# Kernel tuning notes

Measured on AMD Instinct MI355X. Metric: run time of the kernel, lower is better.

Reference implementation:

```python
import jax, jax.numpy as jnp
import numpy as np

C_IN = 256
C_INTER = C_IN // 2  # max(1, C//2)
B, D, H, W = 2, 16, 64, 64


def setup_inputs() -> dict:
    key = jax.random.key(0)
    ks = jax.random.split(key, 9)
    s = 1.0 / np.sqrt(C_IN)
    si = 1.0 / np.sqrt(C_INTER)
    return {
        "x": jax.random.normal(ks[0], (B, C_IN, D, H, W), dtype=jnp.float32),
        # 1x1x1 conv weights reduce to [out, in] matrices
        "g_w": jax.random.normal(ks[1], (C_INTER, C_IN), dtype=jnp.float32) * s,
        "g_b": jax.random.normal(ks[2], (C_INTER,), dtype=jnp.float32) * s,
        "theta_w": jax.random.normal(ks[3], (C_INTER, C_IN), dtype=jnp.float32) * s,
        "theta_b": jax.random.normal(ks[4], (C_INTER,), dtype=jnp.float32) * s,
        "phi_w": jax.random.normal(ks[5], (C_INTER, C_IN), dtype=jnp.float32) * s,
        "phi_b": jax.random.normal(ks[6], (C_INTER,), dtype=jnp.float32) * s,
        # note: torch code inits W to zero; random here so gradients/outputs are non-trivial
        "W_w": jax.random.normal(ks[7], (C_IN, C_INTER), dtype=jnp.float32) * si,
        "W_b": jax.random.normal(ks[8], (C_IN,), dtype=jnp.float32) * si,
    }


def reference(x, g_w, g_b, theta_w, theta_b, phi_w, phi_b, W_w, W_b):
    b, c, d, h, w = x.shape
    n = d * h * w
    xf = x.reshape(b, c, n)  # [B, C, N]
    # 1x1x1 convs == per-position linear projections
    g = jnp.einsum('oc,bcn->bon', g_w, xf) + g_b[None, :, None]        # [B, Ci, N]
    th = jnp.einsum('oc,bcn->bon', theta_w, xf) + theta_b[None, :, None]
    ph = jnp.einsum('oc,bcn->bon', phi_w, xf) + phi_b[None, :, None]
    # f = theta^T @ phi (N x N), y = (f / N) @ g^T. Since the normalizer is a
    # constant, reassociate: kv = phi @ g^T is [Ci, Ci], avoiding the NxN matrix.
    kv = jnp.einsum('bin,bjn->bij', ph, g)                              # [B, Ci, Ci]
    y = jnp.einsum('bin,bij->bjn', th, kv) / n                          # [B, Ci, N]
    y = jnp.einsum('oc,bcn->bon', W_w, y) + W_b[None, :, None]          # [B, C, N]
    return x + y.reshape(b, c, d, h, w)
```

## Files before the change

kernel.cpp:

```cpp
#include <hip/hip_runtime.h>

#define NB 2
#define CC 256
#define CI 128
#define NN 65536
#define KSPLIT 64
#define KCHUNK 1024
#define STAGE 64
#define LDA 72
#define LDX 264

typedef __bf16 bf16x8 __attribute__((ext_vector_type(8)));
typedef float f32x4 __attribute__((ext_vector_type(4)));

__device__ __forceinline__ unsigned short f2bf(float f) {
  unsigned u = __float_as_uint(f);
  u += 0x7fffu + ((u >> 16) & 1u);
  return (unsigned short)(u >> 16);
}

__global__ __launch_bounds__(256) void nl3d_syrk(const float* __restrict__ x,
                                                 float* __restrict__ S,
                                                 float* __restrict__ svec) {
  __shared__ unsigned short ldsA[128 * LDA];
  __shared__ unsigned short ldsB[128 * LDA];
  const int tid = threadIdx.x;
  const int lane = tid & 63;
  const int wv = tid >> 6;
  const int wm = wv >> 1, wn = wv & 1;
  const int b = blockIdx.z;
  const int pair = blockIdx.y;
  const int I = (pair == 2) ? 1 : 0;
  const int J = (pair == 0) ? 0 : 1;
  const bool diag = (I == J);
  const int kc0 = blockIdx.x * KCHUNK;

  const float* xb = x + (size_t)b * CC * NN;
  f32x4 acc[4][4];
  const f32x4 zero4 = {0.f, 0.f, 0.f, 0.f};
#pragma unroll
  for (int i = 0; i < 4; ++i)
#pragma unroll
    for (int j = 0; j < 4; ++j) acc[i][j] = zero4;

  float rsum[8];
#pragma unroll
  for (int i = 0; i < 8; ++i) rsum[i] = 0.f;

  const int rA = tid >> 4;
  const int c4 = tid & 15;
  unsigned short* ldsBp = diag ? ldsA : ldsB;

  for (int s = 0; s < KCHUNK / STAGE; ++s) {
    const int kc = kc0 + s * STAGE;
    float4 fa[8], fb[8];
#pragma unroll
    for (int i = 0; i < 8; ++i) {
      int row = i * 16 + rA;
      fa[i] = *(const float4*)(xb + (size_t)(I * 128 + row) * NN + kc + c4 * 4);
    }
    if (!diag) {
#pragma unroll
      for (int i = 0; i < 8; ++i) {
        int row = i * 16 + rA;
        fb[i] = *(const float4*)(xb + (size_t)(J * 128 + row) * NN + kc + c4 * 4);
      }
    }
    __syncthreads();
#pragma unroll
    for (int i = 0; i < 8; ++i) {
      int row = i * 16 + rA;
      ushort4 h;
      h.x = f2bf(fa[i].x); h.y = f2bf(fa[i].y); h.z = f2bf(fa[i].z); h.w = f2bf(fa[i].w);
      *(ushort4*)&ldsA[row * LDA + c4 * 4] = h;
      if (diag) rsum[i] += fa[i].x + fa[i].y + fa[i].z + fa[i].w;
    }
    if (!diag) {
#pragma unroll
      for (int i = 0; i < 8; ++i) {
        int row = i * 16 + rA;
        ushort4 h;
        h.x = f2bf(fb[i].x); h.y = f2bf(fb[i].y); h.z = f2bf(fb[i].z); h.w = f2bf(fb[i].w);
        *(ushort4*)&ldsB[row * LDA + c4 * 4] = h;
      }
    }
    __syncthreads();

    const int m = lane & 15;
    const int kg = (lane >> 4) * 8;
#pragma unroll
    for (int kk = 0; kk < 2; ++kk) {
      bf16x8 afr[4], bfr[4];
#pragma unroll
      for (int mt = 0; mt < 4; ++mt)
        afr[mt] = *(const bf16x8*)&ldsA[(wm * 64 + mt * 16 + m) * LDA + kk * 32 + kg];
#pragma unroll
      for (int nt = 0; nt < 4; ++nt)
        bfr[nt] = *(const bf16x8*)&ldsBp[(wn * 64 + nt * 16 + m) * LDA + kk * 32 + kg];
#pragma unroll
      for (int mt = 0; mt < 4; ++mt)
#pragma unroll
        for (int nt = 0; nt < 4; ++nt)
          acc[mt][nt] = __builtin_amdgcn_mfma_f32_16x16x32_bf16(afr[mt], bfr[nt], acc[mt][nt], 0, 0, 0);
    }
  }

  {
    float* Sb = S + (size_t)b * CC * CC;
    const int col = lane & 15;
    const int rquad = (lane >> 4) * 4;
#pragma unroll
    for (int mt = 0; mt < 4; ++mt)
#pragma unroll
      for (int nt = 0; nt < 4; ++nt)
#pragma unroll
        for (int r = 0; r < 4; ++r) {
          int gi = I * 128 + wm * 64 + mt * 16 + rquad + r;
          int gj = J * 128 + wn * 64 + nt * 16 + col;
          float v = acc[mt][nt][r];
          atomicAdd(&Sb[gi * CC + gj], v);
          if (!diag) atomicAdd(&Sb[gj * CC + gi], v);
        }
  }

  if (diag) {
    __syncthreads();
    float* ldsRS = (float*)ldsA;
    if (tid < 128) ldsRS[tid] = 0.f;
    __syncthreads();
#pragma unroll
    for (int i = 0; i < 8; ++i) atomicAdd(&ldsRS[i * 16 + rA], rsum[i]);
    __syncthreads();
    if (tid < 128) atomicAdd(&svec[b * CC + I * 128 + tid], ldsRS[tid]);
  }
}

__global__ void nl3d_b0(const float* __restrict__ g_w, float* __restrict__ gwT) {
  int t = blockIdx.x * 256 + threadIdx.x;
  int j = t >> 8, d = t & 255;
  gwT[d * CI + j] = g_w[t];
}

__global__ void nl3d_b1(const float* __restrict__ phi_w, const float* __restrict__ S,
                        float* __restrict__ P) {
  int b = blockIdx.x >> 7, i = blockIdx.x & 127, d = threadIdx.x;
  const float* Sb = S + (size_t)b * CC * CC;
  float acc = 0.f;
  for (int c = 0; c < CC; ++c) acc += phi_w[i * CC + c] * Sb[c * CC + d];
  P[((size_t)b * CI + i) * CC + d] = acc;
}

__global__ void nl3d_b2(const float* __restrict__ P, const float* __restrict__ gwT,
                        const float* __restrict__ svec, const float* __restrict__ phi_w,
                        const float* __restrict__ phi_b, const float* __restrict__ g_b,
                        float* __restrict__ kv) {
  int b = blockIdx.x >> 7, i = blockIdx.x & 127, j = threadIdx.x;
  const float* Pr = P + ((size_t)b * CI + i) * CC;
  const float* sv = svec + b * CC;
  float u = 0.f;
  for (int c = 0; c < CC; ++c) u += phi_w[i * CC + c] * sv[c];
  float acc = 0.f, v = 0.f;
  for (int d = 0; d < CC; ++d) {
    float gT = gwT[d * CI + j];
    acc += Pr[d] * gT;
    v += sv[d] * gT;
  }
  kv[((size_t)b * CI + i) * CI + j] = acc + u * g_b[j] + phi_b[i] * (v + (float)NN * g_b[j]);
}

__global__ void nl3d_b3(const float* __restrict__ kv, const float* __restrict__ theta_w,
                        const float* __restrict__ theta_b, float* __restrict__ T2,
                        float* __restrict__ tb2) {
  int b = blockIdx.x >> 7, j = blockIdx.x & 127, c = threadIdx.x;
  const float* kvb = kv + (size_t)b * CI * CI;
  float acc = 0.f;
  for (int i = 0; i < CI; ++i) acc += kvb[i * CI + j] * theta_w[i * CC + c];
  T2[((size_t)b * CI + j) * CC + c] = acc;
  if (c == 0) {
    float t = 0.f;
    for (int i = 0; i < CI; ++i) t += kvb[i * CI + j] * theta_b[i];
    tb2[b * CI + j] = t;
  }
}

__global__ void nl3d_b4(const float* __restrict__ T2, const float* __restrict__ tb2,
                        const float* __restrict__ W_w, const float* __restrict__ W_b,
                        unsigned short* __restrict__ Mbf, float* __restrict__ cvec) {
  int b = blockIdx.x >> 8, o = blockIdx.x & 255, c = threadIdx.x;
  const float inv = 1.0f / (float)NN;
  float acc = 0.f;
  for (int j = 0; j < CI; ++j) acc += W_w[o * CI + j] * T2[((size_t)b * CI + j) * CC + c];
  Mbf[((size_t)b * CC + o) * CC + c] = f2bf(acc * inv);
  if (c == 0) {
    float t = 0.f;
    for (int j = 0; j < CI; ++j) t += W_w[o * CI + j] * tb2[b * CI + j];
    cvec[b * CC + o] = t * inv + W_b[o];
  }
}

__global__ __launch_bounds__(256) void nl3d_out(const float* __restrict__ x,
                                                const unsigned short* __restrict__ Mbf,
                                                const float* __restrict__ cvec,
                                                float* __restrict__ out) {
  __shared__ unsigned short xT[64 * LDX];
  const int tid = threadIdx.x;
  const int lane = tid & 63;
  const int wv = tid >> 6;
  const int b = blockIdx.y;
  const int n0 = blockIdx.x * 64;

  const float* xb = x + (size_t)b * CC * NN;
  float* ob = out + (size_t)b * CC * NN;

  {
    const int c4 = tid & 15;
#pragma unroll
    for (int i = 0; i < 8; ++i) {
      int p = i * 16 + (tid >> 4);
      float4 f0 = *(const float4*)(xb + (size_t)(2 * p) * NN + n0 + c4 * 4);
      float4 f1 = *(const float4*)(xb + (size_t)(2 * p + 1) * NN + n0 + c4 * 4);
      float a0[4] = {f0.x, f0.y, f0.z, f0.w};
      float a1[4] = {f1.x, f1.y, f1.z, f1.w};
#pragma unroll
      for (int j = 0; j < 4; ++j) {
        unsigned pack = (unsigned)f2bf(a0[j]) | ((unsigned)f2bf(a1[j]) << 16);
        *(unsigned*)&xT[(c4 * 4 + j) * LDX + 2 * p] = pack;
      }
    }
  }
  __syncthreads();

  f32x4 acc[4][4];
  const f32x4 zero4 = {0.f, 0.f, 0.f, 0.f};
#pragma unroll
  for (int i = 0; i < 4; ++i)
#pragma unroll
    for (int j = 0; j < 4; ++j) acc[i][j] = zero4;

  const int m = lane & 15;
  const int kg = (lane >> 4) * 8;
  const unsigned short* Mb = Mbf + (size_t)b * CC * CC;
#pragma unroll
  for (int kc = 0; kc < 8; ++kc) {
    bf16x8 afr[4], bfr[4];
#pragma unroll
    for (int mt = 0; mt < 4; ++mt)
      afr[mt] = *(const bf16x8*)(Mb + (size_t)(wv * 64 + mt * 16 + m) * CC + kc * 32 + kg);
#pragma unroll
    for (int nt = 0; nt < 4; ++nt)
      bfr[nt] = *(const bf16x8*)&xT[(nt * 16 + m) * LDX + kc * 32 + kg];
#pragma unroll
    for (int mt = 0; mt < 4; ++mt)
#pragma unroll
      for (int nt = 0; nt < 4; ++nt)
        acc[mt][nt] = __builtin_amdgcn_mfma_f32_16x16x32_bf16(afr[mt], bfr[nt], acc[mt][nt], 0, 0, 0);
  }

  const int col = lane & 15;
  const int rquad = (lane >> 4) * 4;
#pragma unroll
  for (int mt = 0; mt < 4; ++mt)
#pragma unroll
    for (int r = 0; r < 4; ++r) {
      int o = wv * 64 + mt * 16 + rquad + r;
      float cv = cvec[b * CC + o];
      const float* xrow = xb + (size_t)o * NN + n0;
      float* orow = ob + (size_t)o * NN + n0;
#pragma unroll
      for (int nt = 0; nt < 4; ++nt) {
        int n = nt * 16 + col;
        orow[n] = xrow[n] + acc[mt][nt][r] + cv;
      }
    }
}

extern "C" void kernel_launch(void* const* d_in, const int* in_sizes, int n_in,
                              void* d_out, int out_size, void* d_ws, size_t ws_size,
                              hipStream_t stream) {
  const float* x       = (const float*)d_in[0];
  const float* g_w     = (const float*)d_in[1];
  const float* g_b     = (const float*)d_in[2];
  const float* theta_w = (const float*)d_in[3];
  const float* theta_b = (const float*)d_in[4];
  const float* phi_w   = (const float*)d_in[5];
  const float* phi_b   = (const float*)d_in[6];
  const float* W_w     = (const float*)d_in[7];
  const float* W_b     = (const float*)d_in[8];
  float* out = (float*)d_out;

  char* ws = (char*)d_ws;
  float* S    = (float*)(ws);
  float* svec = (float*)(ws + 524288);
  float* P    = (float*)(ws + 526336);
  float* gwT  = (float*)(ws + 788480);
  float* kv   = (float*)(ws + 919552);
  float* T2   = (float*)(ws + 1050624);
  float* tb2  = (float*)(ws + 1312768);
  unsigned short* Mbf = (unsigned short*)(ws + 1313792);
  float* cvec = (float*)(ws + 1575936);

  hipMemsetAsync(ws, 0, 526336, stream);
  nl3d_syrk<<<dim3(KSPLIT, 3, NB), 256, 0, stream>>>(x, S, svec);
  nl3d_b0<<<128, 256, 0, stream>>>(g_w, gwT);
  nl3d_b1<<<NB * CI, 256, 0, stream>>>(phi_w, S, P);
  nl3d_b2<<<NB * CI, 128, 0, stream>>>(P, gwT, svec, phi_w, phi_b, g_b, kv);
  nl3d_b3<<<NB * CI, 256, 0, stream>>>(kv, theta_w, theta_b, T2, tb2);
  nl3d_b4<<<NB * CC, 256, 0, stream>>>(T2, tb2, W_w, W_b, Mbf, cvec);
  nl3d_out<<<dim3(NN / 64, NB), 256, 0, stream>>>(x, Mbf, cvec, out);
}
```

Baseline: 431.5 us.

## Compute full Gram matrix per block with partial-sum reduction and swizzled LDS

The Gram kernel now computes the full 256x256 product per block with 512 threads, instead of three 128x128 pair blocks, so each x tile is read once per block. When workspace allows, each split writes its partial sum to workspace and a separate kernel reduces them, replacing global atomics. The small matrix kernels use multiple accumulators to break dependency chains, and the output kernel XOR-swizzles its transposed LDS tile to cut bank conflicts. The full-matrix tile computes the symmetric half redundantly, uses more accumulator registers, and adds a partials write/read.

```diff
diff --git a/kernel.cpp b/kernel.cpp
--- a/kernel.cpp
+++ b/kernel.cpp
@@ -4,9 +4,6 @@
 #define CC 256
 #define CI 128
 #define NN 65536
-#define KSPLIT 64
-#define KCHUNK 1024
-#define STAGE 64
 #define LDA 72
 #define LDX 264
 
@@ -19,70 +16,51 @@
   return (unsigned short)(u >> 16);
 }
 
-__global__ __launch_bounds__(256) void nl3d_syrk(const float* __restrict__ x,
-                                                 float* __restrict__ S,
-                                                 float* __restrict__ svec) {
-  __shared__ unsigned short ldsA[128 * LDA];
-  __shared__ unsigned short ldsB[128 * LDA];
+__global__ __launch_bounds__(512) void nl3d_syrk2(const float* __restrict__ x,
+                                                  float* __restrict__ S,
+                                                  float* __restrict__ partials,
+                                                  float* __restrict__ svec,
+                                                  int kchunk, int use_partial) {
+  __shared__ unsigned short lds[256 * LDA];
   const int tid = threadIdx.x;
   const int lane = tid & 63;
   const int wv = tid >> 6;
-  const int wm = wv >> 1, wn = wv & 1;
-  const int b = blockIdx.z;
-  const int pair = blockIdx.y;
-  const int I = (pair == 2) ? 1 : 0;
-  const int J = (pair == 0) ? 0 : 1;
-  const bool diag = (I == J);
-  const int kc0 = blockIdx.x * KCHUNK;
+  const int wm = wv & 3, wn = wv >> 2;
+  const int b = blockIdx.y;
+  const int kc0 = blockIdx.x * kchunk;
 
   const float* xb = x + (size_t)b * CC * NN;
-  f32x4 acc[4][4];
+  f32x4 acc[4][8];
   const f32x4 zero4 = {0.f, 0.f, 0.f, 0.f};
 #pragma unroll
   for (int i = 0; i < 4; ++i)
 #pragma unroll
-    for (int j = 0; j < 4; ++j) acc[i][j] = zero4;
+    for (int j = 0; j < 8; ++j) acc[i][j] = zero4;
 
   float rsum[8];
 #pragma unroll
   for (int i = 0; i < 8; ++i) rsum[i] = 0.f;
 
-  const int rA = tid >> 4;
+  const int r0 = tid >> 4;
   const int c4 = tid & 15;
-  unsigned short* ldsBp = diag ? ldsA : ldsB;
-
-  for (int s = 0; s < KCHUNK / STAGE; ++s) {
-    const int kc = kc0 + s * STAGE;
-    float4 fa[8], fb[8];
+
+  const int stages = kchunk >> 6;
+  for (int s = 0; s < stages; ++s) {
+    const int kc = kc0 + s * 64;
+    float4 f[8];
 #pragma unroll
     for (int i = 0; i < 8; ++i) {
-      int row = i * 16 + rA;
-      fa[i] = *(const float4*)(xb + (size_t)(I * 128 + row) * NN + kc + c4 * 4);
-    }
-    if (!diag) {
-#pragma unroll
-      for (int i = 0; i < 8; ++i) {
-        int row = i * 16 + rA;
-        fb[i] = *(const float4*)(xb + (size_t)(J * 128 + row) * NN + kc + c4 * 4);
-      }
+      int row = r0 + 32 * i;
+      f[i] = *(const float4*)(xb + (size_t)row * NN + kc + c4 * 4);
     }
     __syncthreads();
 #pragma unroll
     for (int i = 0; i < 8; ++i) {
-      int row = i * 16 + rA;
+      int row = r0 + 32 * i;
       ushort4 h;
-      h.x = f2bf(fa[i].x); h.y = f2bf(fa[i].y); h.z = f2bf(fa[i].z); h.w = f2bf(fa[i].w);
-      *(ushort4*)&ldsA[row * LDA + c4 * 4] = h;
-      if (diag) rsum[i] += fa[i].x + fa[i].y + fa[i].z + fa[i].w;
-    }
-    if (!diag) {
-#pragma unroll
-      for (int i = 0; i < 8; ++i) {
-        int row = i * 16 + rA;
-        ushort4 h;
-        h.x = f2bf(fb[i].x); h.y = f2bf(fb[i].y); h.z = f2bf(fb[i].z); h.w = f2bf(fb[i].w);
-        *(ushort4*)&ldsB[row * LDA + c4 * 4] = h;
-      }
+      h.x = f2bf(f[i].x); h.y = f2bf(f[i].y); h.z = f2bf(f[i].z); h.w = f2bf(f[i].w);
+      *(ushort4*)&lds[row * LDA + c4 * 4] = h;
+      rsum[i] += f[i].x + f[i].y + f[i].z + f[i].w;
     }
     __syncthreads();
 
@@ -90,49 +68,76 @@
     const int kg = (lane >> 4) * 8;
 #pragma unroll
     for (int kk = 0; kk < 2; ++kk) {
-      bf16x8 afr[4], bfr[4];
+      bf16x8 afr[4], bfr[8];
 #pragma unroll
       for (int mt = 0; mt < 4; ++mt)
-        afr[mt] = *(const bf16x8*)&ldsA[(wm * 64 + mt * 16 + m) * LDA + kk * 32 + kg];
-#pragma unroll
-      for (int nt = 0; nt < 4; ++nt)
-        bfr[nt] = *(const bf16x8*)&ldsBp[(wn * 64 + nt * 16 + m) * LDA + kk * 32 + kg];
+        afr[mt] = *(const bf16x8*)&lds[(wm * 64 + mt * 16 + m) * LDA + kk * 32 + kg];
+#pragma unroll
+      for (int nt = 0; nt < 8; ++nt)
+        bfr[nt] = *(const bf16x8*)&lds[(wn * 128 + nt * 16 + m) * LDA + kk * 32 + kg];
 #pragma unroll
       for (int mt = 0; mt < 4; ++mt)
 #pragma unroll
-        for (int nt = 0; nt < 4; ++nt)
+        for (int nt = 0; nt < 8; ++nt)
           acc[mt][nt] = __builtin_amdgcn_mfma_f32_16x16x32_bf16(afr[mt], bfr[nt], acc[mt][nt], 0, 0, 0);
     }
   }
 
-  {
+  const int col = lane & 15;
+  const int rq = (lane >> 4) * 4;
+  if (use_partial) {
+    float* dst = partials + ((size_t)(b * gridDim.x + blockIdx.x)) * (CC * CC);
+#pragma unroll
+    for (int mt = 0; mt < 4; ++mt)
+#pragma unroll
+      for (int nt = 0; nt < 8; ++nt)
+#pragma unroll
+        for (int r = 0; r < 4; ++r) {
+          int gi = wm * 64 + mt * 16 + rq + r;
+          int gj = wn * 128 + nt * 16 + col;
+          dst[gi * CC + gj] = acc[mt][nt][r];
+        }
+  } else {
     float* Sb = S + (size_t)b * CC * CC;
-    const int col = lane & 15;
-    const int rquad = (lane >> 4) * 4;
 #pragma unroll
     for (int mt = 0; mt < 4; ++mt)
 #pragma unroll
-      for (int nt = 0; nt < 4; ++nt)
+      for (int nt = 0; nt < 8; ++nt)
 #pragma unroll
         for (int r = 0; r < 4; ++r) {
-          int gi = I * 128 + wm * 64 + mt * 16 + rquad + r;
-          int gj = J * 128 + wn * 64 + nt * 16 + col;
-          float v = acc[mt][nt][r];
-          atomicAdd(&Sb[gi * CC + gj], v);
-          if (!diag) atomicAdd(&Sb[gj * CC + gi], v);
+          int gi = wm * 64 + mt * 16 + rq + r;
+          int gj = wn * 128 + nt * 16 + col;
+          atomicAdd(&Sb[gi * CC + gj], acc[mt][nt][r]);
         }
   }
 
-  if (diag) {
-    __syncthreads();
-    float* ldsRS = (float*)ldsA;
-    if (tid < 128) ldsRS[tid] = 0.f;
-    __syncthreads();
-#pragma unroll
-    for (int i = 0; i < 8; ++i) atomicAdd(&ldsRS[i * 16 + rA], rsum[i]);
-    __syncthreads();
-    if (tid < 128) atomicAdd(&svec[b * CC + I * 128 + tid], ldsRS[tid]);
-  }
+  __syncthreads();
+  float* ldsRS = (float*)lds;
+  if (tid < 256) ldsRS[tid] = 0.f;
+  __syncthreads();
+#pragma unroll
+  for (int i = 0; i < 8; ++i) atomicAdd(&ldsRS[r0 + 32 * i], rsum[i]);
+  __syncthreads();
+  if (tid < 256) atomicAdd(&svec[b * CC + tid], ldsRS[tid]);
+}
+
+__global__ __launch_bounds__(256) void nl3d_reduce(const float* __restrict__ partials,
+                                                   float* __restrict__ S, int splits) {
+  const int e = blockIdx.x * 256 + threadIdx.x;
+  const int b = e >> 14;
+  const int off = e & 16383;
+  const float4* p = (const float4*)partials;
+  float4 a0 = {0, 0, 0, 0}, a1 = {0, 0, 0, 0};
+  const size_t base = (size_t)b * splits * 16384 + off;
+  for (int s = 0; s < splits; s += 2) {
+    float4 v0 = p[base + (size_t)s * 16384];
+    float4 v1 = p[base + (size_t)(s + 1) * 16384];
+    a0.x += v0.x; a0.y += v0.y; a0.z += v0.z; a0.w += v0.w;
+    a1.x += v1.x; a1.y += v1.y; a1.z += v1.z; a1.w += v1.w;
+  }
+  float4 r;
+  r.x = a0.x + a1.x; r.y = a0.y + a1.y; r.z = a0.z + a1.z; r.w = a0.w + a1.w;
+  ((float4*)S)[e] = r;
 }
 
 __global__ void nl3d_b0(const float* __restrict__ g_w, float* __restrict__ gwT) {
@@ -145,9 +150,15 @@
                         float* __restrict__ P) {
   int b = blockIdx.x >> 7, i = blockIdx.x & 127, d = threadIdx.x;
   const float* Sb = S + (size_t)b * CC * CC;
-  float acc = 0.f;
-  for (int c = 0; c < CC; ++c) acc += phi_w[i * CC + c] * Sb[c * CC + d];
-  P[((size_t)b * CI + i) * CC + d] = acc;
+  const float* ph = phi_w + i * CC;
+  float a0 = 0.f, a1 = 0.f, a2 = 0.f, a3 = 0.f;
+  for (int c = 0; c < CC; c += 4) {
+    a0 += ph[c + 0] * Sb[(c + 0) * CC + d];
+    a1 += ph[c + 1] * Sb[(c + 1) * CC + d];
+    a2 += ph[c + 2] * Sb[(c + 2) * CC + d];
+    a3 += ph[c + 3] * Sb[(c + 3) * CC + d];
+  }
+  P[((size_t)b * CI + i) * CC + d] = (a0 + a1) + (a2 + a3);
 }
 
 __global__ void nl3d_b2(const float* __restrict__ P, const float* __restrict__ gwT,
@@ -157,15 +168,20 @@
   int b = blockIdx.x >> 7, i = blockIdx.x & 127, j = threadIdx.x;
   const float* Pr = P + ((size_t)b * CI + i) * CC;
   const float* sv = svec + b * CC;
-  float u = 0.f;
-  for (int c = 0; c < CC; ++c) u += phi_w[i * CC + c] * sv[c];
-  float acc = 0.f, v = 0.f;
-  for (int d = 0; d < CC; ++d) {
-    float gT = gwT[d * CI + j];
-    acc += Pr[d] * gT;
-    v += sv[d] * gT;
-  }
-  kv[((size_t)b * CI + i) * CI + j] = acc + u * g_b[j] + phi_b[i] * (v + (float)NN * g_b[j]);
+  const float* ph = phi_w + i * CC;
+  float u0 = 0.f, u1 = 0.f;
+  for (int c = 0; c < CC; c += 2) {
+    u0 += ph[c] * sv[c];
+    u1 += ph[c + 1] * sv[c + 1];
+  }
+  float a0 = 0.f, a1 = 0.f, v0 = 0.f, v1 = 0.f;
+  for (int d = 0; d < CC; d += 2) {
+    float gT0 = gwT[d * CI + j], gT1 = gwT[(d + 1) * CI + j];
+    a0 += Pr[d] * gT0; a1 += Pr[d + 1] * gT1;
+    v0 += sv[d] * gT0; v1 += sv[d + 1] * gT1;
+  }
+  kv[((size_t)b * CI + i) * CI + j] =
+      (a0 + a1) + (u0 + u1) * g_b[j] + phi_b[i] * ((v0 + v1) + (float)NN * g_b[j]);
 }
 
 __global__ void nl3d_b3(const float* __restrict__ kv, const float* __restrict__ theta_w,
@@ -173,9 +189,12 @@
                         float* __restrict__ tb2) {
   int b = blockIdx.x >> 7, j = blockIdx.x & 127, c = threadIdx.x;
   const float* kvb = kv + (size_t)b * CI * CI;
-  float acc = 0.f;
-  for (int i = 0; i < CI; ++i) acc += kvb[i * CI + j] * theta_w[i * CC + c];
-  T2[((size_t)b * CI + j) * CC + c] = acc;
+  float a0 = 0.f, a1 = 0.f;
+  for (int i = 0; i < CI; i += 2) {
+    a0 += kvb[i * CI + j] * theta_w[i * CC + c];
+    a1 += kvb[(i + 1) * CI + j] * theta_w[(i + 1) * CC + c];
+  }
+  T2[((size_t)b * CI + j) * CC + c] = a0 + a1;
   if (c == 0) {
     float t = 0.f;
     for (int i = 0; i < CI; ++i) t += kvb[i * CI + j] * theta_b[i];
@@ -188,12 +207,16 @@
                         unsigned short* __restrict__ Mbf, float* __restrict__ cvec) {
   int b = blockIdx.x >> 8, o = blockIdx.x & 255, c = threadIdx.x;
   const float inv = 1.0f / (float)NN;
-  float acc = 0.f;
-  for (int j = 0; j < CI; ++j) acc += W_w[o * CI + j] * T2[((size_t)b * CI + j) * CC + c];
-  Mbf[((size_t)b * CC + o) * CC + c] = f2bf(acc * inv);
+  const float* Wr = W_w + o * CI;
+  float a0 = 0.f, a1 = 0.f;
+  for (int j = 0; j < CI; j += 2) {
+    a0 += Wr[j] * T2[((size_t)b * CI + j) * CC + c];
+    a1 += Wr[j + 1] * T2[((size_t)b * CI + j + 1) * CC + c];
+  }
+  Mbf[((size_t)b * CC + o) * CC + c] = f2bf((a0 + a1) * inv);
   if (c == 0) {
     float t = 0.f;
-    for (int j = 0; j < CI; ++j) t += W_w[o * CI + j] * tb2[b * CI + j];
+    for (int j = 0; j < CI; ++j) t += Wr[j] * tb2[b * CI + j];
     cvec[b * CC + o] = t * inv + W_b[o];
   }
 }
@@ -221,10 +244,11 @@
       float4 f1 = *(const float4*)(xb + (size_t)(2 * p + 1) * NN + n0 + c4 * 4);
       float a0[4] = {f0.x, f0.y, f0.z, f0.w};
       float a1[4] = {f1.x, f1.y, f1.z, f1.w};
+      int ps = p ^ ((c4 & 7) << 2);
 #pragma unroll
       for (int j = 0; j < 4; ++j) {
         unsigned pack = (unsigned)f2bf(a0[j]) | ((unsigned)f2bf(a1[j]) << 16);
-        *(unsigned*)&xT[(c4 * 4 + j) * LDX + 2 * p] = pack;
+        *(unsigned*)&xT[(c4 * 4 + j) * LDX + 2 * ps] = pack;
       }
     }
   }
@@ -247,8 +271,11 @@
     for (int mt = 0; mt < 4; ++mt)
       afr[mt] = *(const bf16x8*)(Mb + (size_t)(wv * 64 + mt * 16 + m) * CC + kc * 32 + kg);
 #pragma unroll
-    for (int nt = 0; nt < 4; ++nt)
-      bfr[nt] = *(const bf16x8*)&xT[(nt * 16 + m) * LDX + kc * 32 + kg];
+    for (int nt = 0; nt < 4; ++nt) {
+      int rr = nt * 16 + m;
+      int d0 = (kc * 16 + (kg >> 1)) ^ (((rr >> 2) & 7) << 2);
+      bfr[nt] = *(const bf16x8*)&xT[rr * LDX + 2 * d0];
+    }
 #pragma unroll
     for (int mt = 0; mt < 4; ++mt)
 #pragma unroll
@@ -298,9 +325,23 @@
   float* tb2  = (float*)(ws + 1312768);
   unsigned short* Mbf = (unsigned short*)(ws + 1313792);
   float* cvec = (float*)(ws + 1575936);
-
-  hipMemsetAsync(ws, 0, 526336, stream);
-  nl3d_syrk<<<dim3(KSPLIT, 3, NB), 256, 0, stream>>>(x, S, svec);
+  float* partials = (float*)(ws + 2097152);
+
+  int splits = 0;
+  for (int c = 128; c >= 8; c >>= 1) {
+    if (2097152 + (size_t)NB * c * CC * CC * 4 <= ws_size) { splits = c; break; }
+  }
+
+  if (splits > 0) {
+    hipMemsetAsync(svec, 0, 2048, stream);
+    nl3d_syrk2<<<dim3(splits, NB), 512, 0, stream>>>(x, S, partials, svec,
+                                                     NN / splits, 1);
+    nl3d_reduce<<<128, 256, 0, stream>>>(partials, S, splits);
+  } else {
+    hipMemsetAsync(ws, 0, 526336, stream);
+    nl3d_syrk2<<<dim3(64, NB), 512, 0, stream>>>(x, S, (float*)ws, svec,
+                                                 NN / 64, 0);
+  }
   nl3d_b0<<<128, 256, 0, stream>>>(g_w, gwT);
   nl3d_b1<<<NB * CI, 256, 0, stream>>>(phi_w, S, P);
   nl3d_b2<<<NB * CI, 128, 0, stream>>>(P, gwT, svec, phi_w, phi_b, g_b, kv);
```

Result: faster. 394.4 us (-8.6%).
